# Optimization experiments

Hardware: AMD Instinct MI355X
Metric: run time of the kernel (lower is better)

## Reference

```python
import jax, jax.numpy as jnp
import numpy as np

B, S, D = 4, 2048, 1024
E = 8            # num_experts
F = 4096         # expert hidden dim (4*D)
T = B * S        # tokens
CAP = 1280       # capacity = ceil(1.25 * T / E)


def setup_inputs() -> dict:
    key = jax.random.key(0)
    k1, k2, k3, k4 = jax.random.split(key, 4)
    inputs = jax.random.normal(k1, (B, S, D), dtype=jnp.float32)
    gate_w = jax.random.normal(k2, (D, E), dtype=jnp.float32) / np.sqrt(D)
    w1 = jax.random.normal(k3, (E, D, F), dtype=jnp.float32) / np.sqrt(D)
    w2 = jax.random.normal(k4, (E, F, D), dtype=jnp.float32) / np.sqrt(F)
    return {"inputs": inputs, "gate_w": gate_w, "w1": w1, "w2": w2}


def reference(inputs, gate_w, w1, w2):
    tokens = inputs.reshape(-1, D)                       # [T, D]
    logits = tokens @ gate_w                             # [T, E] (gate, no bias)
    probs = jax.nn.softmax(logits, axis=-1)
    expert_idx = jnp.argmax(probs, axis=-1)              # top-1 routing
    mask1 = jax.nn.one_hot(expert_idx, E, dtype=tokens.dtype)        # [T, E]
    # position of each token within its chosen expert's queue
    pos = (jnp.cumsum(mask1, axis=0) - 1.0).astype(jnp.int32)        # [T, E]
    # one_hot of out-of-range (>= CAP) positions is all-zero -> capacity drop
    sec_mask = mask1[:, :, None] * jax.nn.one_hot(pos, CAP, dtype=tokens.dtype)  # [T, E, C]
    combine_weights = probs[:, :, None] * sec_mask       # [T, E, C]
    # dispatch: matmul(sec_mask.permute(1,2,0), tokens) -> [E, C, D]
    expert_input = jnp.einsum('tec,td->ecd', sec_mask, tokens)
    # grouped per-expert FFN
    h = jax.nn.relu(jnp.einsum('ecd,edf->ecf', expert_input, w1))    # [E, C, F]
    expert_output = jnp.einsum('ecf,efd->ecd', h, w2)                # [E, C, D]
    # combine: [T, E*C] @ [E*C, D]
    out = jnp.einsum('tec,ecd->td', combine_weights, expert_output)  # [T, D]
    return out.reshape(inputs.shape)
```

## Files before the change

kernel.cpp:

```cpp
#include <hip/hip_runtime.h>
#include <hip/hip_bf16.h>

#define TOKENS   8192
#define DDIM     1024
#define NEXP     8
#define FDIM     4096
#define CAPACITY 1280
#define NYT      10

typedef __attribute__((ext_vector_type(8))) __bf16 bf16x8;
typedef __attribute__((ext_vector_type(4))) __bf16 bf16x4;
typedef __attribute__((ext_vector_type(4))) float  f32x4;

typedef __attribute__((address_space(1))) const void gvoid_t;
typedef __attribute__((address_space(3))) void       lvoid_t;

__device__ __forceinline__ void async16(const void* g, void* l) {
  __builtin_amdgcn_global_load_lds((gvoid_t*)g, (lvoid_t*)l, 16, 0, 0);
}

__global__ void gate_kernel(const float* __restrict__ x, const float* __restrict__ gw,
                            int* __restrict__ eidx, float* __restrict__ prob) {
  const int t = blockIdx.x;
  const int lane = threadIdx.x;
  const float* xp = x + (size_t)t * DDIM;
  float acc[NEXP];
#pragma unroll
  for (int e = 0; e < NEXP; ++e) acc[e] = 0.f;
#pragma unroll 4
  for (int i = 0; i < DDIM / 64; ++i) {
    const int d = i * 64 + lane;
    const float xv = xp[d];
    const f32x4 g0 = *(const f32x4*)(gw + d * NEXP);
    const f32x4 g1 = *(const f32x4*)(gw + d * NEXP + 4);
    acc[0] += xv * g0[0]; acc[1] += xv * g0[1];
    acc[2] += xv * g0[2]; acc[3] += xv * g0[3];
    acc[4] += xv * g1[0]; acc[5] += xv * g1[1];
    acc[6] += xv * g1[2]; acc[7] += xv * g1[3];
  }
#pragma unroll
  for (int e = 0; e < NEXP; ++e) {
    float v = acc[e];
#pragma unroll
    for (int off = 32; off; off >>= 1) v += __shfl_xor(v, off);
    acc[e] = v;
  }
  if (lane == 0) {
    float m = acc[0]; int mi = 0;
#pragma unroll
    for (int e = 1; e < NEXP; ++e) if (acc[e] > m) { m = acc[e]; mi = e; }
    float s = 0.f;
#pragma unroll
    for (int e = 0; e < NEXP; ++e) s += __expf(acc[e] - m);
    eidx[t] = mi;
    prob[t] = 1.f / s;
  }
}

__global__ void scan_kernel(const int* __restrict__ eidx, int* __restrict__ src,
                            int* __restrict__ counts) {
  __shared__ int buf[2][NEXP][256];
  const int tid = threadIdx.x;
  for (int i = tid; i < NEXP * CAPACITY; i += 256) src[i] = -1;
  const int t0 = tid * (TOKENS / 256);
#pragma unroll
  for (int e = 0; e < NEXP; ++e) buf[0][e][tid] = 0;
  for (int k = 0; k < TOKENS / 256; ++k) {
    const int e = eidx[t0 + k];
    buf[0][e][tid]++;
  }
  __syncthreads();
  int cur = 0;
  for (int off = 1; off < 256; off <<= 1) {
#pragma unroll
    for (int e = 0; e < NEXP; ++e) {
      int v = buf[cur][e][tid];
      if (tid >= off) v += buf[cur][e][tid - off];
      buf[cur ^ 1][e][tid] = v;
    }
    __syncthreads();
    cur ^= 1;
  }
  if (tid < NEXP) counts[tid] = buf[cur][tid][255];
#pragma unroll
  for (int e = 0; e < NEXP; ++e)
    buf[cur ^ 1][e][tid] = (tid > 0) ? buf[cur][e][tid - 1] : 0;
  for (int k = 0; k < TOKENS / 256; ++k) {
    const int t = t0 + k;
    const int e = eidx[t];
    const int p = buf[cur ^ 1][e][tid]++;
    if (p < CAPACITY) src[e * CAPACITY + p] = t;
  }
}

__global__ void dispatch_kernel(const float* __restrict__ tokens, const int* __restrict__ src,
                                __bf16* __restrict__ Xb) {
  const int slot = blockIdx.x;
  const int tid  = threadIdx.x;
  const int t = src[slot];
  bf16x4* dst = (bf16x4*)(Xb + (size_t)slot * DDIM);
  bf16x4 o;
  if (t >= 0) {
    const f32x4 v = ((const f32x4*)(tokens + (size_t)t * DDIM))[tid];
    o[0] = (__bf16)v[0]; o[1] = (__bf16)v[1]; o[2] = (__bf16)v[2]; o[3] = (__bf16)v[3];
  } else {
    o[0] = (__bf16)0.f; o[1] = (__bf16)0.f; o[2] = (__bf16)0.f; o[3] = (__bf16)0.f;
  }
  dst[tid] = o;
}

__global__ void transpose_convert_kernel(const float* __restrict__ w, __bf16* __restrict__ wt,
                                         int R, int C) {
  __shared__ __bf16 tile[64][66];
  const int e = blockIdx.z;
  const float* wp = w + (size_t)e * R * C;
  __bf16* op = wt + (size_t)e * R * C;
  const int c0 = blockIdx.x * 64, r0 = blockIdx.y * 64;
  const int tid = threadIdx.x;
#pragma unroll
  for (int p = 0; p < 4; ++p) {
    const int r = p * 16 + (tid >> 4);
    const int c = (tid & 15) * 4;
    const f32x4 v = *(const f32x4*)(wp + (size_t)(r0 + r) * C + c0 + c);
    tile[r][c]     = (__bf16)v[0]; tile[r][c + 1] = (__bf16)v[1];
    tile[r][c + 2] = (__bf16)v[2]; tile[r][c + 3] = (__bf16)v[3];
  }
  __syncthreads();
#pragma unroll
  for (int p = 0; p < 2; ++p) {
    const int c  = p * 32 + (tid >> 3);
    const int rg = (tid & 7) * 8;
    bf16x8 o;
#pragma unroll
    for (int i = 0; i < 8; ++i) o[i] = tile[rg + i][c];
    *(bf16x8*)(op + (size_t)(c0 + c) * R + r0 + rg) = o;
  }
}

template <int MODE>
__global__ __launch_bounds__(256, 2)
void gemm_kernel(const __bf16* __restrict__ A, const __bf16* __restrict__ B,
                 __bf16* __restrict__ Cbf, float* __restrict__ out,
                 const int* __restrict__ src, const float* __restrict__ prob,
                 const int* __restrict__ counts,
                 int K, size_t sA, size_t sB, size_t sC) {
  constexpr int N  = (MODE == 0) ? FDIM : DDIM;
  constexpr int NX = N / 128;
  __shared__ __bf16 lds[2][128 * 64];

  const int nwg = NX * NYT * NEXP;
  int wg = blockIdx.x;
  wg = (wg & 7) * (nwg >> 3) + (wg >> 3);
  const int e   = wg / (NX * NYT);
  const int rem = wg - e * (NX * NYT);
  const int ty  = rem % NYT;
  const int tx  = rem / NYT;
  const int m0  = ty * 128, n0 = tx * 128;

  const int cnt   = counts[e];
  const int tiles = (cnt + 127) >> 7;
  if (ty >= ((tiles < NYT) ? tiles : NYT)) return;

  const __bf16* Ae = A + (size_t)e * sA;
  const __bf16* Be = B + (size_t)e * sB;
  const int tid = threadIdx.x;
  const int wid = tid >> 6, lane = tid & 63;
  const int wm = wid >> 1, wn = wid & 1;
  const int rl = lane & 15, gl = lane >> 4;

  f32x4 acc[4][4];
#pragma unroll
  for (int m = 0; m < 4; ++m)
#pragma unroll
    for (int n = 0; n < 4; ++n) acc[m][n] = (f32x4){0.f, 0.f, 0.f, 0.f};

  for (int kt = 0; kt < K; kt += 64) {
#pragma unroll
    for (int i = 0; i < 4; ++i) {
      const int s   = (wid * 4 + i) * 64 + lane;
      const int row = s >> 3;
      const int cg  = (s & 7) ^ (row & 7);
      async16(Ae + (size_t)(m0 + row) * K + kt + cg * 8, &lds[0][(wid * 4 + i) * 512]);
      async16(Be + (size_t)(n0 + row) * K + kt + cg * 8, &lds[1][(wid * 4 + i) * 512]);
    }
    __syncthreads();
    const char* la = (const char*)&lds[0][0];
    const char* lb = (const char*)&lds[1][0];
#pragma unroll
    for (int kk = 0; kk < 2; ++kk) {
      bf16x8 af[4], bv[4];
#pragma unroll
      for (int m = 0; m < 4; ++m) {
        const int rowin = wm * 64 + m * 16 + rl;
        af[m] = *(const bf16x8*)(la + rowin * 128 + (((kk * 4 + gl) ^ (rowin & 7)) * 16));
      }
#pragma unroll
      for (int n = 0; n < 4; ++n) {
        const int rowin = wn * 64 + n * 16 + rl;
        bv[n] = *(const bf16x8*)(lb + rowin * 128 + (((kk * 4 + gl) ^ (rowin & 7)) * 16));
      }
#pragma unroll
      for (int m = 0; m < 4; ++m)
#pragma unroll
        for (int n = 0; n < 4; ++n)
          acc[m][n] = __builtin_amdgcn_mfma_f32_16x16x32_bf16(af[m], bv[n], acc[m][n], 0, 0, 0);
    }
    __syncthreads();
  }

  if (MODE == 0) {
    __bf16* Ce = Cbf + (size_t)e * sC;
#pragma unroll
    for (int m = 0; m < 4; ++m)
#pragma unroll
      for (int j = 0; j < 4; ++j) {
        const int row = m0 + wm * 64 + m * 16 + gl * 4 + j;
#pragma unroll
        for (int n = 0; n < 4; ++n) {
          const int col = n0 + wn * 64 + n * 16 + rl;
          float v = acc[m][n][j];
          v = v > 0.f ? v : 0.f;
          Ce[(size_t)row * N + col] = (__bf16)v;
        }
      }
  } else {
#pragma unroll
    for (int m = 0; m < 4; ++m)
#pragma unroll
      for (int j = 0; j < 4; ++j) {
        const int slot = m0 + wm * 64 + m * 16 + gl * 4 + j;
        const int t = src[e * CAPACITY + slot];
        if (t >= 0) {
          const float p = prob[t];
          float* op = out + (size_t)t * N;
#pragma unroll
          for (int n = 0; n < 4; ++n) {
            const int col = n0 + wn * 64 + n * 16 + rl;
            op[col] = p * acc[m][n][j];
          }
        }
      }
  }
}

extern "C" void kernel_launch(void* const* d_in, const int* in_sizes, int n_in,
                              void* d_out, int out_size, void* d_ws, size_t ws_size,
                              hipStream_t stream) {
  const float* x  = (const float*)d_in[0];
  const float* gw = (const float*)d_in[1];
  const float* w1 = (const float*)d_in[2];
  const float* w2 = (const float*)d_in[3];
  float* out = (float*)d_out;

  char* ws = (char*)d_ws;
  size_t off = 0;
  auto alloc = [&](size_t bytes) {
    void* p = ws + off;
    off += (bytes + 255) & ~(size_t)255;
    return p;
  };
  __bf16* W1bT = (__bf16*)alloc((size_t)NEXP * FDIM * DDIM * 2);
  __bf16* W2bT = (__bf16*)alloc((size_t)NEXP * DDIM * FDIM * 2);
  __bf16* Xb   = (__bf16*)alloc((size_t)NEXP * CAPACITY * DDIM * 2);
  __bf16* Hb   = (__bf16*)alloc((size_t)NEXP * CAPACITY * FDIM * 2);
  int*   eidx  = (int*)alloc(TOKENS * sizeof(int));
  float* prob  = (float*)alloc(TOKENS * sizeof(float));
  int*   srcm  = (int*)alloc(NEXP * CAPACITY * sizeof(int));
  int*   cnts  = (int*)alloc(NEXP * sizeof(int));
  (void)ws_size; (void)in_sizes; (void)n_in;

  hipMemsetAsync(d_out, 0, (size_t)out_size * sizeof(float), stream);

  gate_kernel<<<TOKENS, 64, 0, stream>>>(x, gw, eidx, prob);
  scan_kernel<<<1, 256, 0, stream>>>(eidx, srcm, cnts);
  dispatch_kernel<<<NEXP * CAPACITY, 256, 0, stream>>>(x, srcm, Xb);
  transpose_convert_kernel<<<dim3(FDIM / 64, DDIM / 64, NEXP), 256, 0, stream>>>(
      w1, W1bT, DDIM, FDIM);
  transpose_convert_kernel<<<dim3(DDIM / 64, FDIM / 64, NEXP), 256, 0, stream>>>(
      w2, W2bT, FDIM, DDIM);
  gemm_kernel<0><<<(FDIM / 128) * NYT * NEXP, 256, 0, stream>>>(
      Xb, W1bT, Hb, nullptr, nullptr, nullptr, cnts,
      DDIM, (size_t)CAPACITY * DDIM, (size_t)FDIM * DDIM, (size_t)CAPACITY * FDIM);
  gemm_kernel<1><<<(DDIM / 128) * NYT * NEXP, 256, 0, stream>>>(
      Hb, W2bT, nullptr, out, srcm, prob, cnts,
      FDIM, (size_t)CAPACITY * FDIM, (size_t)DDIM * FDIM, 0);
}
```

Before: 326.5 us.

## Fuse fp32 weight transpose and bf16 conversion into GEMM B-tile loading

Removes the two separate transpose/convert kernels and the bf16 weight buffers in the workspace. Each GEMM now reads the original fp32 expert weights directly with vector global loads, converts them to bf16 in registers, and writes them transposed into LDS. The LDS swizzle gains an extra XOR term so these stores and the MFMA fragment reads avoid bank conflicts. This cuts a full extra pass of reading and writing the weights. In exchange, every M tile re-reads the weights at fp32 width, and the B loads are now synchronous register loads with no async prefetch, so more load latency sits in the GEMM main loop.

```diff
diff --git a/kernel.cpp b/kernel.cpp
--- a/kernel.cpp
+++ b/kernel.cpp
@@ -109,41 +109,13 @@
   dst[tid] = o;
 }
 
-__global__ void transpose_convert_kernel(const float* __restrict__ w, __bf16* __restrict__ wt,
-                                         int R, int C) {
-  __shared__ __bf16 tile[64][66];
-  const int e = blockIdx.z;
-  const float* wp = w + (size_t)e * R * C;
-  __bf16* op = wt + (size_t)e * R * C;
-  const int c0 = blockIdx.x * 64, r0 = blockIdx.y * 64;
-  const int tid = threadIdx.x;
-#pragma unroll
-  for (int p = 0; p < 4; ++p) {
-    const int r = p * 16 + (tid >> 4);
-    const int c = (tid & 15) * 4;
-    const f32x4 v = *(const f32x4*)(wp + (size_t)(r0 + r) * C + c0 + c);
-    tile[r][c]     = (__bf16)v[0]; tile[r][c + 1] = (__bf16)v[1];
-    tile[r][c + 2] = (__bf16)v[2]; tile[r][c + 3] = (__bf16)v[3];
-  }
-  __syncthreads();
-#pragma unroll
-  for (int p = 0; p < 2; ++p) {
-    const int c  = p * 32 + (tid >> 3);
-    const int rg = (tid & 7) * 8;
-    bf16x8 o;
-#pragma unroll
-    for (int i = 0; i < 8; ++i) o[i] = tile[rg + i][c];
-    *(bf16x8*)(op + (size_t)(c0 + c) * R + r0 + rg) = o;
-  }
-}
-
 template <int MODE>
 __global__ __launch_bounds__(256, 2)
-void gemm_kernel(const __bf16* __restrict__ A, const __bf16* __restrict__ B,
+void gemm_kernel(const __bf16* __restrict__ A, const float* __restrict__ Bw,
                  __bf16* __restrict__ Cbf, float* __restrict__ out,
                  const int* __restrict__ src, const float* __restrict__ prob,
                  const int* __restrict__ counts,
-                 int K, size_t sA, size_t sB, size_t sC) {
+                 int K, size_t sA, size_t sBw, size_t sC) {
   constexpr int N  = (MODE == 0) ? FDIM : DDIM;
   constexpr int NX = N / 128;
   __shared__ __bf16 lds[2][128 * 64];
@@ -162,11 +134,13 @@
   if (ty >= ((tiles < NYT) ? tiles : NYT)) return;
 
   const __bf16* Ae = A + (size_t)e * sA;
-  const __bf16* Be = B + (size_t)e * sB;
+  const float*  Be = Bw + (size_t)e * sBw;
   const int tid = threadIdx.x;
   const int wid = tid >> 6, lane = tid & 63;
   const int wm = wid >> 1, wn = wid & 1;
   const int rl = lane & 15, gl = lane >> 4;
+  const int nq = tid & 31;
+  const int kb = tid >> 5;
 
   f32x4 acc[4][4];
 #pragma unroll
@@ -175,13 +149,25 @@
     for (int n = 0; n < 4; ++n) acc[m][n] = (f32x4){0.f, 0.f, 0.f, 0.f};
 
   for (int kt = 0; kt < K; kt += 64) {
+    f32x4 r[8];
+#pragma unroll
+    for (int i = 0; i < 8; ++i)
+      r[i] = *(const f32x4*)(Be + (size_t)(kt + kb * 8 + i) * N + n0 + nq * 4);
 #pragma unroll
     for (int i = 0; i < 4; ++i) {
       const int s   = (wid * 4 + i) * 64 + lane;
       const int row = s >> 3;
       const int cg  = (s & 7) ^ (row & 7);
       async16(Ae + (size_t)(m0 + row) * K + kt + cg * 8, &lds[0][(wid * 4 + i) * 512]);
-      async16(Be + (size_t)(n0 + row) * K + kt + cg * 8, &lds[1][(wid * 4 + i) * 512]);
+    }
+#pragma unroll
+    for (int i2 = 0; i2 < 4; ++i2) {
+      const int n  = nq * 4 + i2;
+      const int sl = kb ^ (n & 7) ^ ((n >> 3) & 7);
+      bf16x8 o;
+#pragma unroll
+      for (int i = 0; i < 8; ++i) o[i] = (__bf16)r[i][i2];
+      *(bf16x8*)((char*)&lds[1][0] + n * 128 + sl * 16) = o;
     }
     __syncthreads();
     const char* la = (const char*)&lds[0][0];
@@ -197,7 +183,8 @@
 #pragma unroll
       for (int n = 0; n < 4; ++n) {
         const int rowin = wn * 64 + n * 16 + rl;
-        bv[n] = *(const bf16x8*)(lb + rowin * 128 + (((kk * 4 + gl) ^ (rowin & 7)) * 16));
+        const int sl = (kk * 4 + gl) ^ (rowin & 7) ^ ((rowin >> 3) & 7);
+        bv[n] = *(const bf16x8*)(lb + rowin * 128 + sl * 16);
       }
 #pragma unroll
       for (int m = 0; m < 4; ++m)
@@ -259,8 +246,6 @@
     off += (bytes + 255) & ~(size_t)255;
     return p;
   };
-  __bf16* W1bT = (__bf16*)alloc((size_t)NEXP * FDIM * DDIM * 2);
-  __bf16* W2bT = (__bf16*)alloc((size_t)NEXP * DDIM * FDIM * 2);
   __bf16* Xb   = (__bf16*)alloc((size_t)NEXP * CAPACITY * DDIM * 2);
   __bf16* Hb   = (__bf16*)alloc((size_t)NEXP * CAPACITY * FDIM * 2);
   int*   eidx  = (int*)alloc(TOKENS * sizeof(int));
@@ -274,14 +259,10 @@
   gate_kernel<<<TOKENS, 64, 0, stream>>>(x, gw, eidx, prob);
   scan_kernel<<<1, 256, 0, stream>>>(eidx, srcm, cnts);
   dispatch_kernel<<<NEXP * CAPACITY, 256, 0, stream>>>(x, srcm, Xb);
-  transpose_convert_kernel<<<dim3(FDIM / 64, DDIM / 64, NEXP), 256, 0, stream>>>(
-      w1, W1bT, DDIM, FDIM);
-  transpose_convert_kernel<<<dim3(DDIM / 64, FDIM / 64, NEXP), 256, 0, stream>>>(
-      w2, W2bT, FDIM, DDIM);
   gemm_kernel<0><<<(FDIM / 128) * NYT * NEXP, 256, 0, stream>>>(
-      Xb, W1bT, Hb, nullptr, nullptr, nullptr, cnts,
-      DDIM, (size_t)CAPACITY * DDIM, (size_t)FDIM * DDIM, (size_t)CAPACITY * FDIM);
+      Xb, w1, Hb, nullptr, nullptr, nullptr, cnts,
+      DDIM, (size_t)CAPACITY * DDIM, (size_t)DDIM * FDIM, (size_t)CAPACITY * FDIM);
   gemm_kernel<1><<<(DDIM / 128) * NYT * NEXP, 256, 0, stream>>>(
-      Hb, W2bT, nullptr, out, srcm, prob, cnts,
-      FDIM, (size_t)CAPACITY * FDIM, (size_t)DDIM * FDIM, 0);
-}
+      Hb, w2, nullptr, out, srcm, prob, cnts,
+      FDIM, (size_t)CAPACITY * FDIM, (size_t)FDIM * DDIM, 0);
+}
```

New measurement: 330.8 us. Within noise of the previous version (+1.3%).

## Fuse w2 fp32-to-bf16 transpose into second expert GEMM B-tile load

Applied to the files above, without the earlier changes.

Drops the separate transpose/convert pass over w2 and has the second GEMM read the fp32 weights directly. Each iteration loads them into registers, converts them to bf16 and writes them transposed into swizzled LDS. This removes a full write and re-read of the bf16 copy of w2. In exchange each GEMM2 workgroup reads fp32 weights, twice the bytes, and up to ten row tiles per expert re-read the same weights. The B load is also now synchronous rather than async-to-LDS, so there is less latency overlap.

```diff
diff --git a/kernel.cpp b/kernel.cpp
--- a/kernel.cpp
+++ b/kernel.cpp
@@ -137,14 +137,11 @@
   }
 }
 
-template <int MODE>
 __global__ __launch_bounds__(256, 2)
-void gemm_kernel(const __bf16* __restrict__ A, const __bf16* __restrict__ B,
-                 __bf16* __restrict__ Cbf, float* __restrict__ out,
-                 const int* __restrict__ src, const float* __restrict__ prob,
-                 const int* __restrict__ counts,
-                 int K, size_t sA, size_t sB, size_t sC) {
-  constexpr int N  = (MODE == 0) ? FDIM : DDIM;
+void gemm1_kernel(const __bf16* __restrict__ A, const __bf16* __restrict__ B,
+                  __bf16* __restrict__ Cbf, const int* __restrict__ counts,
+                  int K, size_t sA, size_t sB, size_t sC) {
+  constexpr int N  = FDIM;
   constexpr int NX = N / 128;
   __shared__ __bf16 lds[2][128 * 64];
 
@@ -208,39 +205,122 @@
     __syncthreads();
   }
 
-  if (MODE == 0) {
-    __bf16* Ce = Cbf + (size_t)e * sC;
-#pragma unroll
-    for (int m = 0; m < 4; ++m)
-#pragma unroll
-      for (int j = 0; j < 4; ++j) {
-        const int row = m0 + wm * 64 + m * 16 + gl * 4 + j;
+  __bf16* Ce = Cbf + (size_t)e * sC;
+#pragma unroll
+  for (int m = 0; m < 4; ++m)
+#pragma unroll
+    for (int j = 0; j < 4; ++j) {
+      const int row = m0 + wm * 64 + m * 16 + gl * 4 + j;
+#pragma unroll
+      for (int n = 0; n < 4; ++n) {
+        const int col = n0 + wn * 64 + n * 16 + rl;
+        float v = acc[m][n][j];
+        v = v > 0.f ? v : 0.f;
+        Ce[(size_t)row * N + col] = (__bf16)v;
+      }
+    }
+}
+
+__global__ __launch_bounds__(256, 2)
+void gemm2_kernel(const __bf16* __restrict__ A, const float* __restrict__ Bw,
+                  float* __restrict__ out, const int* __restrict__ src,
+                  const float* __restrict__ prob, const int* __restrict__ counts,
+                  int K, size_t sA, size_t sBw) {
+  constexpr int N  = DDIM;
+  constexpr int NX = N / 128;
+  __shared__ __bf16 lds[2][128 * 64];
+
+  const int nwg = NX * NYT * NEXP;
+  int wg = blockIdx.x;
+  wg = (wg & 7) * (nwg >> 3) + (wg >> 3);
+  const int e   = wg / (NX * NYT);
+  const int rem = wg - e * (NX * NYT);
+  const int ty  = rem % NYT;
+  const int tx  = rem / NYT;
+  const int m0  = ty * 128, n0 = tx * 128;
+
+  const int cnt   = counts[e];
+  const int tiles = (cnt + 127) >> 7;
+  if (ty >= ((tiles < NYT) ? tiles : NYT)) return;
+
+  const __bf16* Ae = A + (size_t)e * sA;
+  const float*  Be = Bw + (size_t)e * sBw;
+  const int tid = threadIdx.x;
+  const int wid = tid >> 6, lane = tid & 63;
+  const int wm = wid >> 1, wn = wid & 1;
+  const int rl = lane & 15, gl = lane >> 4;
+  const int nq = tid & 31;
+  const int kb = tid >> 5;
+
+  f32x4 acc[4][4];
+#pragma unroll
+  for (int m = 0; m < 4; ++m)
+#pragma unroll
+    for (int n = 0; n < 4; ++n) acc[m][n] = (f32x4){0.f, 0.f, 0.f, 0.f};
+
+  for (int kt = 0; kt < K; kt += 64) {
+    f32x4 r[8];
+#pragma unroll
+    for (int i = 0; i < 8; ++i)
+      r[i] = *(const f32x4*)(Be + (size_t)(kt + kb * 8 + i) * N + n0 + nq * 4);
+#pragma unroll
+    for (int i = 0; i < 4; ++i) {
+      const int s   = (wid * 4 + i) * 64 + lane;
+      const int row = s >> 3;
+      const int cg  = (s & 7) ^ (row & 7);
+      async16(Ae + (size_t)(m0 + row) * K + kt + cg * 8, &lds[0][(wid * 4 + i) * 512]);
+    }
+#pragma unroll
+    for (int i2 = 0; i2 < 4; ++i2) {
+      const int n  = nq * 4 + i2;
+      const int sl = kb ^ (n & 7) ^ ((n >> 3) & 7);
+      bf16x8 o;
+#pragma unroll
+      for (int i = 0; i < 8; ++i) o[i] = (__bf16)r[i][i2];
+      *(bf16x8*)((char*)&lds[1][0] + n * 128 + sl * 16) = o;
+    }
+    __syncthreads();
+    const char* la = (const char*)&lds[0][0];
+    const char* lb = (const char*)&lds[1][0];
+#pragma unroll
+    for (int kk = 0; kk < 2; ++kk) {
+      bf16x8 af[4], bv[4];
+#pragma unroll
+      for (int m = 0; m < 4; ++m) {
+        const int rowin = wm * 64 + m * 16 + rl;
+        af[m] = *(const bf16x8*)(la + rowin * 128 + (((kk * 4 + gl) ^ (rowin & 7)) * 16));
+      }
+#pragma unroll
+      for (int n = 0; n < 4; ++n) {
+        const int rowin = wn * 64 + n * 16 + rl;
+        const int sl = (kk * 4 + gl) ^ (rowin & 7) ^ ((rowin >> 3) & 7);
+        bv[n] = *(const bf16x8*)(lb + rowin * 128 + sl * 16);
+      }
+#pragma unroll
+      for (int m = 0; m < 4; ++m)
+#pragma unroll
+        for (int n = 0; n < 4; ++n)
+          acc[m][n] = __builtin_amdgcn_mfma_f32_16x16x32_bf16(af[m], bv[n], acc[m][n], 0, 0, 0);
+    }
+    __syncthreads();
+  }
+
+#pragma unroll
+  for (int m = 0; m < 4; ++m)
+#pragma unroll
+    for (int j = 0; j < 4; ++j) {
+      const int slot = m0 + wm * 64 + m * 16 + gl * 4 + j;
+      const int t = src[e * CAPACITY + slot];
+      if (t >= 0) {
+        const float p = prob[t];
+        float* op = out + (size_t)t * N;
 #pragma unroll
         for (int n = 0; n < 4; ++n) {
           const int col = n0 + wn * 64 + n * 16 + rl;
-          float v = acc[m][n][j];
-          v = v > 0.f ? v : 0.f;
-          Ce[(size_t)row * N + col] = (__bf16)v;
+          op[col] = p * acc[m][n][j];
         }
       }
-  } else {
-#pragma unroll
-    for (int m = 0; m < 4; ++m)
-#pragma unroll
-      for (int j = 0; j < 4; ++j) {
-        const int slot = m0 + wm * 64 + m * 16 + gl * 4 + j;
-        const int t = src[e * CAPACITY + slot];
-        if (t >= 0) {
-          const float p = prob[t];
-          float* op = out + (size_t)t * N;
-#pragma unroll
-          for (int n = 0; n < 4; ++n) {
-            const int col = n0 + wn * 64 + n * 16 + rl;
-            op[col] = p * acc[m][n][j];
-          }
-        }
-      }
-  }
+    }
 }
 
 extern "C" void kernel_launch(void* const* d_in, const int* in_sizes, int n_in,
@@ -260,7 +340,6 @@
     return p;
   };
   __bf16* W1bT = (__bf16*)alloc((size_t)NEXP * FDIM * DDIM * 2);
-  __bf16* W2bT = (__bf16*)alloc((size_t)NEXP * DDIM * FDIM * 2);
   __bf16* Xb   = (__bf16*)alloc((size_t)NEXP * CAPACITY * DDIM * 2);
   __bf16* Hb   = (__bf16*)alloc((size_t)NEXP * CAPACITY * FDIM * 2);
   int*   eidx  = (int*)alloc(TOKENS * sizeof(int));
@@ -276,12 +355,10 @@
   dispatch_kernel<<<NEXP * CAPACITY, 256, 0, stream>>>(x, srcm, Xb);
   transpose_convert_kernel<<<dim3(FDIM / 64, DDIM / 64, NEXP), 256, 0, stream>>>(
       w1, W1bT, DDIM, FDIM);
-  transpose_convert_kernel<<<dim3(DDIM / 64, FDIM / 64, NEXP), 256, 0, stream>>>(
-      w2, W2bT, FDIM, DDIM);
-  gemm_kernel<0><<<(FDIM / 128) * NYT * NEXP, 256, 0, stream>>>(
-      Xb, W1bT, Hb, nullptr, nullptr, nullptr, cnts,
+  gemm1_kernel<<<(FDIM / 128) * NYT * NEXP, 256, 0, stream>>>(
+      Xb, W1bT, Hb, cnts,
       DDIM, (size_t)CAPACITY * DDIM, (size_t)FDIM * DDIM, (size_t)CAPACITY * FDIM);
-  gemm_kernel<1><<<(DDIM / 128) * NYT * NEXP, 256, 0, stream>>>(
-      Hb, W2bT, nullptr, out, srcm, prob, cnts,
-      FDIM, (size_t)CAPACITY * FDIM, (size_t)DDIM * FDIM, 0);
-}
+  gemm2_kernel<<<(DDIM / 128) * NYT * NEXP, 256, 0, stream>>>(
+      Hb, w2, out, srcm, prob, cnts,
+      FDIM, (size_t)CAPACITY * FDIM, (size_t)FDIM * DDIM);
+}
```

After: 305.0 us (median of 2 runs). 6.6% less time.
